# Kernel optimization log

Hardware: AMD Instinct MI355X
Metric: run time of the kernel (lower is better)

The kernel has to match this reference:

```python
import jax, jax.numpy as jnp
import numpy as np

B, L, E, H, D, OUT = 4, 2048, 1024, 8, 128, 1024


def setup_inputs() -> dict:
    key = jax.random.key(0)
    ks = jax.random.split(key, 6)
    stdv = 1.0 / np.sqrt(D)
    return {
        "k": jax.random.normal(ks[0], (B, L, E), dtype=jnp.float32),
        "q": jax.random.normal(ks[1], (B, L, E), dtype=jnp.float32),
        "w_kx": jax.random.uniform(ks[2], (H, E, D), minval=-stdv, maxval=stdv, dtype=jnp.float32),
        "w_qx": jax.random.uniform(ks[3], (H, E, D), minval=-stdv, maxval=stdv, dtype=jnp.float32),
        "proj_w": jax.random.normal(ks[4], (OUT, H * D), dtype=jnp.float32) * 0.02,
        "proj_b": jnp.zeros((OUT,), dtype=jnp.float32),
        "flag": False,
    }


def reference(k, q, w_kx, w_qx, proj_w, proj_b, flag):
    # Per-head sigmoid projections, vectorized over heads (original loops over heads).
    d = w_kx.shape[-1]
    kx = jax.nn.sigmoid(jnp.einsum('ble,hed->bhld', k, w_kx))  # [B,H,Lk,D]
    if flag:
        # flag==True: q is used directly (already hidden_dim-sized), shared across heads
        qx = jnp.broadcast_to(q[:, None], (q.shape[0], kx.shape[1], q.shape[1], q.shape[2]))
    else:
        qx = jax.nn.sigmoid(jnp.einsum('bqe,hed->bhqd', q, w_qx))  # [B,H,Lq,D]
    # scaled dot-product score + softmax over key axis
    score = jnp.einsum('bhqd,bhkd->bhqk', qx, kx) * (1.0 / jnp.sqrt(jnp.asarray(d, kx.dtype)))
    attn = jax.nn.softmax(score, axis=-1)
    out = jnp.einsum('bhqk,bhkd->bhqd', attn, kx)  # [B,H,Lq,D]
    # concat heads along feature dim, then linear projection (dropout p=0 -> identity)
    b, h, lq, _ = out.shape
    out = out.transpose(0, 2, 1, 3).reshape(b, lq, h * d)
    return out @ proj_w.T + proj_b
```

## Files before the change

### kernel.cpp

```cpp
#include <hip/hip_runtime.h>

#define BB 4
#define LL 2048
#define EE 1024
#define HH 8
#define DD 128
#define OO 1024
#define MM (BB*LL)
#define ND (HH*DD)

#define QBLK 128
#define KVBLK 64
#define NT (LL / KVBLK)

#define C2 0.12751920678739807f

typedef __bf16 bf16;
typedef unsigned short u16;
typedef __bf16 bf16x8 __attribute__((ext_vector_type(8)));
typedef __bf16 bf16x4 __attribute__((ext_vector_type(4)));
typedef float  f32x4  __attribute__((ext_vector_type(4)));

__device__ __forceinline__ void gl16(const bf16* g, bf16* l) {
#if __has_builtin(__builtin_amdgcn_global_load_lds)
    __builtin_amdgcn_global_load_lds((const __attribute__((address_space(1))) char*)g,
                                     (__attribute__((address_space(3))) char*)l, 16, 0, 0);
#else
    *(bf16x8*)l = *(const bf16x8*)g;
#endif
}

__device__ __forceinline__ bf16x8 cvt8(const float* s) {
    float4 f0 = *(const float4*)s;
    float4 f1 = *(const float4*)(s + 4);
    bf16x8 v;
    v[0] = (bf16)f0.x; v[1] = (bf16)f0.y; v[2] = (bf16)f0.z; v[3] = (bf16)f0.w;
    v[4] = (bf16)f1.x; v[5] = (bf16)f1.y; v[6] = (bf16)f1.z; v[7] = (bf16)f1.w;
    return v;
}

__global__ void detect_kernel(const u16* __restrict__ data, int* __restrict__ mode) {
    if (threadIdx.x == 0 && blockIdx.x == 0) {
        int cnt = 0;
        for (int i = 0; i < 512; i++) {
            int e = (data[i] >> 7) & 0xFF;
            if (e >= 117 && e <= 132) cnt++;
        }
        *mode = (cnt > 400) ? 1 : 0;
    }
}

__global__ __launch_bounds__(256) void fill_kernel(float* __restrict__ out, float v, int n) {
    int i = blockIdx.x * 256 + threadIdx.x;
    if (i < n) out[i] = v;
}

__global__ __launch_bounds__(256) void wtrans_kernel(const void* __restrict__ in0,
                                                     const void* __restrict__ in1,
                                                     bf16* __restrict__ outT0,
                                                     bf16* __restrict__ outT1,
                                                     const int* __restrict__ mode) {
    const void* in = blockIdx.y ? in1 : in0;
    bf16* outT = blockIdx.y ? outT1 : outT0;
    int idx = blockIdx.x * 256 + threadIdx.x;
    int i4 = idx * 4;
    int h = i4 >> 17;
    int rem = i4 & 131071;
    int e = rem >> 7;
    int d = rem & 127;
    size_t ob = ((size_t)h * DD + d) * EE + e;
    if (*mode) {
        bf16x4 v = *(const bf16x4*)((const bf16*)in + i4);
        outT[ob]          = v[0];
        outT[ob + EE]     = v[1];
        outT[ob + 2 * EE] = v[2];
        outT[ob + 3 * EE] = v[3];
    } else {
        float4 v = *(const float4*)((const float*)in + i4);
        outT[ob]          = (bf16)v.x;
        outT[ob + EE]     = (bf16)v.y;
        outT[ob + 2 * EE] = (bf16)v.z;
        outT[ob + 3 * EE] = (bf16)v.w;
    }
}

__global__ __launch_bounds__(256) void gemm_kernel(const void* __restrict__ A0,
                                                   const void* __restrict__ A1,
                                                   const void* __restrict__ BT0,
                                                   const void* __restrict__ BT1,
                                                   bf16* __restrict__ outBF0,
                                                   bf16* __restrict__ outBF1,
                                                   bf16* __restrict__ outT,
                                                   float* __restrict__ outF,
                                                   const void* __restrict__ PB,
                                                   const int* __restrict__ mode,
                                                   const int epi) {
    __shared__ __align__(16) bf16 As[128 * 64];
    __shared__ __align__(16) bf16 Bs[128 * 64];
    const int md = *mode;
    const int aBf = (epi == 2) ? 1 : md;
    const int bBf = (epi == 2) ? md : 1;
    const int t = threadIdx.x;
    const int w = t >> 6, l = t & 63;
    const int lr = l & 15, lg = l >> 4;
    const int wr = w >> 1, wc = w & 1;
    const int o = blockIdx.x + (blockIdx.y << 3);
    const int half = (epi == 3) ? (o >> 9) : 0;
    const int oo = o & 511;
    const int mt = (oo & 7) * 8 + ((oo >> 3) & 7);
    const int ntile = oo >> 6;
    const int m0 = mt * 128, n0 = ntile * 128;
    const void* A = half ? A1 : A0;
    const void* BT = half ? BT1 : BT0;

    f32x4 acc[4][4];
    const f32x4 zero = {0.f, 0.f, 0.f, 0.f};
#pragma unroll
    for (int i = 0; i < 4; i++)
#pragma unroll
        for (int j = 0; j < 4; j++) acc[i][j] = zero;

    for (int kt = 0; kt < 16; ++kt) {
        const int k0 = kt * 64;
        __syncthreads();
        if (aBf) {
#pragma unroll
            for (int p = 0; p < 4; p++) {
                const int id = p * 256 + t;
                const int row = id >> 3;
                const int c = (id & 7) ^ (row & 7);
                gl16((const bf16*)A + (size_t)(m0 + row) * 1024 + k0 + c * 8,
                     As + (p * 256 + w * 64) * 8);
            }
        } else {
#pragma unroll
            for (int p = 0; p < 4; p++) {
                const int id = p * 256 + t;
                const int row = id >> 3;
                const int cc = id & 7;
                bf16x8 v = cvt8((const float*)A + (size_t)(m0 + row) * 1024 + k0 + cc * 8);
                *(bf16x8*)(As + row * 64 + ((cc ^ (row & 7)) << 3)) = v;
            }
        }
        if (bBf) {
#pragma unroll
            for (int p = 0; p < 4; p++) {
                const int id = p * 256 + t;
                const int row = id >> 3;
                const int c = (id & 7) ^ (row & 7);
                gl16((const bf16*)BT + (size_t)(n0 + row) * 1024 + k0 + c * 8,
                     Bs + (p * 256 + w * 64) * 8);
            }
        } else {
#pragma unroll
            for (int p = 0; p < 4; p++) {
                const int id = p * 256 + t;
                const int row = id >> 3;
                const int cc = id & 7;
                bf16x8 v = cvt8((const float*)BT + (size_t)(n0 + row) * 1024 + k0 + cc * 8);
                *(bf16x8*)(Bs + row * 64 + ((cc ^ (row & 7)) << 3)) = v;
            }
        }
        __syncthreads();
        bf16x8 af[4][2], bg[4][2];
#pragma unroll
        for (int i = 0; i < 4; i++) {
            const int ar = wr * 64 + i * 16 + lr;
#pragma unroll
            for (int ks = 0; ks < 2; ks++)
                af[i][ks] = *(const bf16x8*)(As + ar * 64 + (((ks * 4 + lg) ^ (ar & 7)) << 3));
        }
#pragma unroll
        for (int j = 0; j < 4; j++) {
            const int br = wc * 64 + j * 16 + lr;
#pragma unroll
            for (int ks = 0; ks < 2; ks++)
                bg[j][ks] = *(const bf16x8*)(Bs + br * 64 + (((ks * 4 + lg) ^ (br & 7)) << 3));
        }
#pragma unroll
        for (int i = 0; i < 4; i++)
#pragma unroll
            for (int j = 0; j < 4; j++) {
                acc[i][j] = __builtin_amdgcn_mfma_f32_16x16x32_bf16(af[i][0], bg[j][0], acc[i][j], 0, 0, 0);
                acc[i][j] = __builtin_amdgcn_mfma_f32_16x16x32_bf16(af[i][1], bg[j][1], acc[i][j], 0, 0, 0);
            }
    }

    if (epi == 3) {
        bf16* outBF = half ? outBF1 : outBF0;
        const float mulf = half ? C2 : 1.0f;
        const int b_idx = m0 >> 11;
        const int h = n0 >> 7;
#pragma unroll
        for (int i = 0; i < 4; i++) {
#pragma unroll
            for (int j = 0; j < 4; j++) {
                const int gr = m0 + wr * 64 + i * 16 + lg * 4;
                const int gc = n0 + wc * 64 + j * 16 + lr;
                float s0 = mulf / (1.0f + __expf(-acc[i][j][0]));
                float s1 = mulf / (1.0f + __expf(-acc[i][j][1]));
                float s2 = mulf / (1.0f + __expf(-acc[i][j][2]));
                float s3 = mulf / (1.0f + __expf(-acc[i][j][3]));
                outBF[(size_t)gr * ND + gc]           = (bf16)s0;
                outBF[(size_t)(gr + 1) * ND + gc]     = (bf16)s1;
                outBF[(size_t)(gr + 2) * ND + gc]     = (bf16)s2;
                outBF[(size_t)(gr + 3) * ND + gc]     = (bf16)s3;
                if (!half) {
                    bf16x4 pk;
                    pk[0] = (bf16)s0; pk[1] = (bf16)s1; pk[2] = (bf16)s2; pk[3] = (bf16)s3;
                    const int d = gc & 127;
                    const int lrow = gr & 2047;
                    *(bf16x4*)(outT + (((size_t)(h * BB + b_idx)) * DD + d) * LL + lrow) = pk;
                }
            }
        }
    } else {
#pragma unroll
        for (int j = 0; j < 4; j++) {
            const int gc = n0 + wc * 64 + j * 16 + lr;
            const float bias = md ? (float)((const bf16*)PB)[gc] : ((const float*)PB)[gc];
#pragma unroll
            for (int i = 0; i < 4; i++) {
                const int gr = m0 + wr * 64 + i * 16 + lg * 4;
#pragma unroll
                for (int reg = 0; reg < 4; reg++)
                    outF[(size_t)(gr + reg) * OO + gc] = acc[i][j][reg] + bias;
            }
        }
    }
}

__global__ __launch_bounds__(512, 4) void attn_kernel(const bf16* __restrict__ QX,
                                                      const bf16* __restrict__ KX,
                                                      const bf16* __restrict__ KXT,
                                                      bf16* __restrict__ AO) {
    __shared__ __align__(16) bf16 Kl[2][KVBLK * 128];
    __shared__ __align__(16) bf16 Vt[2][128 * KVBLK];
    __shared__ __align__(16) bf16 Pl[8][16 * 64];
    const int t = threadIdx.x;
    const int w = t >> 6, l = t & 63;
    const int lr = l & 15, lg = l >> 4;
    const int bid = blockIdx.x;
    const int orig = (bid & 7) * 64 + (bid >> 3);
    const int bh = orig >> 4;
    const int h = bh & 7, b = bh >> 3;
    const int q0 = (orig & 15) * QBLK;
    const bf16* qxh = QX + (size_t)(b * LL) * ND + h * DD;
    const bf16* kxh = KX + (size_t)(b * LL) * ND + h * DD;
    const bf16* kxt = KXT + ((size_t)(h * BB + b)) * DD * LL;

    const int kid1 = 512 + t;
    const int krow0 = t >> 4,    kcc0 = t & 15;
    const int krow1 = kid1 >> 4, kcc1 = kid1 & 15;
    const int vrow0 = t >> 3,    vcc0 = t & 7;
    const int vrow1 = kid1 >> 3, vcc1 = kid1 & 7;
    const bf16* kp0 = kxh + (size_t)krow0 * ND + kcc0 * 8;
    const bf16* kp1 = kxh + (size_t)krow1 * ND + kcc1 * 8;
    const bf16* vp0 = kxt + (size_t)vrow0 * LL + vcc0 * 8;
    const bf16* vp1 = kxt + (size_t)vrow1 * LL + vcc1 * 8;
    const int kw0 = krow0 * 128 + ((kcc0 ^ (krow0 & 15)) << 3);
    const int kw1 = krow1 * 128 + ((kcc1 ^ (krow1 & 15)) << 3);
    const int vw0 = vrow0 * 64 + ((vcc0 ^ (vrow0 & 7)) << 3);
    const int vw1 = vrow1 * 64 + ((vcc1 ^ (vrow1 & 7)) << 3);

    bf16x8 qf[4];
    const int qrow = q0 + w * 16 + lr;
#pragma unroll
    for (int s = 0; s < 4; s++)
        qf[s] = *(const bf16x8*)(qxh + (size_t)qrow * ND + s * 32 + lg * 8);

    bf16x8 rk0 = *(const bf16x8*)(kp0);
    bf16x8 rk1 = *(const bf16x8*)(kp1);
    bf16x8 rv0 = *(const bf16x8*)(vp0);
    bf16x8 rv1 = *(const bf16x8*)(vp1);
    *(bf16x8*)(Kl[0] + kw0) = rk0;
    *(bf16x8*)(Kl[0] + kw1) = rk1;
    *(bf16x8*)(Vt[0] + vw0) = rv0;
    *(bf16x8*)(Vt[0] + vw1) = rv1;
    rk0 = *(const bf16x8*)(kp0 + (size_t)KVBLK * ND);
    rk1 = *(const bf16x8*)(kp1 + (size_t)KVBLK * ND);
    rv0 = *(const bf16x8*)(vp0 + KVBLK);
    rv1 = *(const bf16x8*)(vp1 + KVBLK);
    __syncthreads();

    f32x4 oacc[8];
    const f32x4 zero = {0.f, 0.f, 0.f, 0.f};
#pragma unroll
    for (int n = 0; n < 8; n++) oacc[n] = zero;
    float psum = 0.f;

    for (int kt = 0; kt < NT; ++kt) {
        const int cur = kt & 1;
        if (kt + 1 < NT) {
            *(bf16x8*)(Kl[cur ^ 1] + kw0) = rk0;
            *(bf16x8*)(Kl[cur ^ 1] + kw1) = rk1;
            *(bf16x8*)(Vt[cur ^ 1] + vw0) = rv0;
            *(bf16x8*)(Vt[cur ^ 1] + vw1) = rv1;
            if (kt + 2 < NT) {
                const size_t ko = (size_t)(kt + 2) * KVBLK * ND;
                const int vo = (kt + 2) * KVBLK;
                rk0 = *(const bf16x8*)(kp0 + ko);
                rk1 = *(const bf16x8*)(kp1 + ko);
                rv0 = *(const bf16x8*)(vp0 + vo);
                rv1 = *(const bf16x8*)(vp1 + vo);
            }
        }
        const bf16* KlC = Kl[cur];
        const bf16* VtC = Vt[cur];

        f32x4 sa[4];
        __builtin_amdgcn_s_setprio(1);
#pragma unroll
        for (int n = 0; n < 4; n++) {
            sa[n] = zero;
#pragma unroll
            for (int ks = 0; ks < 4; ks++) {
                int arow = n * 16 + lr;
                bf16x8 kb = *(const bf16x8*)(KlC + arow * 128 + ((((ks * 4 + lg) ^ (arow & 15))) << 3));
                sa[n] = __builtin_amdgcn_mfma_f32_16x16x32_bf16(kb, qf[ks], sa[n], 0, 0, 0);
            }
        }
        __builtin_amdgcn_s_setprio(0);
#pragma unroll
        for (int n = 0; n < 4; n++) {
            bf16x4 pk;
#pragma unroll
            for (int j = 0; j < 4; j++) {
                float p = exp2f(sa[n][j]);
                psum += p;
                pk[j] = (bf16)p;
            }
            const int chunk = (2 * n + (lg >> 1)) ^ (lr & 7);
            *(bf16x4*)(Pl[w] + lr * 64 + chunk * 8 + (lg & 1) * 4) = pk;
        }
        asm volatile("s_waitcnt lgkmcnt(0)" ::: "memory");
        __builtin_amdgcn_sched_barrier(0);
        bf16x8 pb0 = *(const bf16x8*)(Pl[w] + lr * 64 + (((lg ^ (lr & 7))) << 3));
        bf16x8 pb1 = *(const bf16x8*)(Pl[w] + lr * 64 + ((((4 + lg) ^ (lr & 7))) << 3));
        __builtin_amdgcn_s_setprio(1);
#pragma unroll
        for (int n = 0; n < 8; n++) {
            int vrow = n * 16 + lr;
            bf16x8 vb0 = *(const bf16x8*)(VtC + vrow * 64 + (((lg ^ (vrow & 7))) << 3));
            oacc[n] = __builtin_amdgcn_mfma_f32_16x16x32_bf16(vb0, pb0, oacc[n], 0, 0, 0);
            bf16x8 vb1 = *(const bf16x8*)(VtC + vrow * 64 + ((((4 + lg) ^ (vrow & 7))) << 3));
            oacc[n] = __builtin_amdgcn_mfma_f32_16x16x32_bf16(vb1, pb1, oacc[n], 0, 0, 0);
        }
        __builtin_amdgcn_s_setprio(0);
        __syncthreads();
    }
    float tot = psum;
    tot += __shfl_xor(tot, 16);
    tot += __shfl_xor(tot, 32);
    const float linv = 1.0f / tot;
    const int arow = b * LL + q0 + w * 16 + lr;
    bf16* aoRow = AO + (size_t)arow * ND + h * DD;
#pragma unroll
    for (int n = 0; n < 8; n++) {
        bf16x4 o;
#pragma unroll
        for (int reg = 0; reg < 4; reg++) o[reg] = (bf16)(oacc[n][reg] * linv);
        *(bf16x4*)(aoRow + n * 16 + lg * 4) = o;
    }
}

extern "C" void kernel_launch(void* const* d_in, const int* in_sizes, int n_in,
                              void* d_out, int out_size, void* d_ws, size_t ws_size,
                              hipStream_t stream) {
    (void)in_sizes; (void)n_in;
    float* out = (float*)d_out;

    const size_t NEED = ((size_t)(2 + 2 + 16 + 16 + 16 + 16) << 20) + 256;
    if (ws_size < NEED) {
        hipLaunchKernelGGL(fill_kernel, dim3((out_size + 255) / 256), dim3(256), 0, stream,
                           out, (float)(ws_size >> 20), out_size);
        return;
    }

    int* mode = (int*)d_ws;
    bf16* base = (bf16*)((char*)d_ws + 256);
    bf16* wkT = base;
    bf16* wqT = wkT + (size_t)HH * DD * EE;
    bf16* kx  = wqT + (size_t)HH * DD * EE;
    bf16* qx  = kx  + (size_t)MM * ND;
    bf16* kxT = qx  + (size_t)MM * ND;
    bf16* ao  = kxT + (size_t)HH * MM * DD;

    hipLaunchKernelGGL(detect_kernel, dim3(1), dim3(64), 0, stream, (const u16*)d_in[0], mode);
    hipLaunchKernelGGL(wtrans_kernel, dim3(HH * EE * DD / 4 / 256, 2), dim3(256), 0, stream,
                       d_in[2], d_in[3], wkT, wqT, mode);
    hipLaunchKernelGGL(gemm_kernel, dim3(8, 128), dim3(256), 0, stream,
                       d_in[0], d_in[1], wkT, wqT, kx, qx, kxT,
                       (float*)nullptr, (const void*)nullptr, mode, 3);
    hipLaunchKernelGGL(attn_kernel, dim3(512), dim3(512), 0, stream, qx, kx, kxT, ao);
    hipLaunchKernelGGL(gemm_kernel, dim3(8, 64), dim3(256), 0, stream,
                       ao, (const void*)nullptr, d_in[4], (const void*)nullptr,
                       (bf16*)nullptr, (bf16*)nullptr, (bf16*)nullptr, out, d_in[5], mode, 2);
}
```

Before: 199.4 us.

## Halve attention query block to 64 rows and single-buffer K/V in LDS

The attention kernel now processes 64 query rows per block with 4 waves instead of 128 rows with 8, doubling the grid to 1024 blocks. The K/V LDS staging drops double buffering in favor of a single buffer with register prefetch and two barriers per tile, and the P scratch swizzle is changed to a 4-element granularity. The aim is to cut LDS use per block and raise occupancy. In exchange, each K/V tile is reloaded by twice as many blocks and the extra barrier exposes more synchronization.

Result: slower. 249.3 us (+25.1%).

```diff
diff --git a/kernel.cpp b/kernel.cpp
--- a/kernel.cpp
+++ b/kernel.cpp
@@ -9,7 +9,7 @@
 #define MM (BB*LL)
 #define ND (HH*DD)
 
-#define QBLK 128
+#define QBLK 64
 #define KVBLK 64
 #define NT (LL / KVBLK)
 
@@ -230,38 +230,38 @@
     }
 }
 
-__global__ __launch_bounds__(512, 4) void attn_kernel(const bf16* __restrict__ QX,
+__global__ __launch_bounds__(256, 4) void attn_kernel(const bf16* __restrict__ QX,
                                                       const bf16* __restrict__ KX,
                                                       const bf16* __restrict__ KXT,
                                                       bf16* __restrict__ AO) {
-    __shared__ __align__(16) bf16 Kl[2][KVBLK * 128];
-    __shared__ __align__(16) bf16 Vt[2][128 * KVBLK];
-    __shared__ __align__(16) bf16 Pl[8][16 * 64];
+    __shared__ __align__(16) bf16 Kl[KVBLK * 128];
+    __shared__ __align__(16) bf16 Vt[128 * KVBLK];
+    __shared__ __align__(16) bf16 Pl[4][16 * 64];
     const int t = threadIdx.x;
     const int w = t >> 6, l = t & 63;
     const int lr = l & 15, lg = l >> 4;
     const int bid = blockIdx.x;
-    const int orig = (bid & 7) * 64 + (bid >> 3);
-    const int bh = orig >> 4;
+    const int orig = (bid & 7) * 128 + (bid >> 3);
+    const int bh = orig >> 5;
     const int h = bh & 7, b = bh >> 3;
-    const int q0 = (orig & 15) * QBLK;
+    const int q0 = (orig & 31) * QBLK;
     const bf16* qxh = QX + (size_t)(b * LL) * ND + h * DD;
     const bf16* kxh = KX + (size_t)(b * LL) * ND + h * DD;
     const bf16* kxt = KXT + ((size_t)(h * BB + b)) * DD * LL;
 
-    const int kid1 = 512 + t;
-    const int krow0 = t >> 4,    kcc0 = t & 15;
-    const int krow1 = kid1 >> 4, kcc1 = kid1 & 15;
-    const int vrow0 = t >> 3,    vcc0 = t & 7;
-    const int vrow1 = kid1 >> 3, vcc1 = kid1 & 7;
-    const bf16* kp0 = kxh + (size_t)krow0 * ND + kcc0 * 8;
-    const bf16* kp1 = kxh + (size_t)krow1 * ND + kcc1 * 8;
-    const bf16* vp0 = kxt + (size_t)vrow0 * LL + vcc0 * 8;
-    const bf16* vp1 = kxt + (size_t)vrow1 * LL + vcc1 * 8;
-    const int kw0 = krow0 * 128 + ((kcc0 ^ (krow0 & 15)) << 3);
-    const int kw1 = krow1 * 128 + ((kcc1 ^ (krow1 & 15)) << 3);
-    const int vw0 = vrow0 * 64 + ((vcc0 ^ (vrow0 & 7)) << 3);
-    const int vw1 = vrow1 * 64 + ((vcc1 ^ (vrow1 & 7)) << 3);
+    const bf16* kpK[4];
+    const bf16* kpV[4];
+    int kw[4], vw[4];
+#pragma unroll
+    for (int p = 0; p < 4; p++) {
+        const int id = p * 256 + t;
+        const int krow = id >> 4, kcc = id & 15;
+        kpK[p] = kxh + (size_t)krow * ND + kcc * 8;
+        kw[p] = krow * 128 + ((kcc ^ (krow & 15)) << 3);
+        const int vrow = id >> 3, vcc = id & 7;
+        kpV[p] = kxt + (size_t)vrow * LL + vcc * 8;
+        vw[p] = vrow * 64 + ((vcc ^ (vrow & 7)) << 3);
+    }
 
     bf16x8 qf[4];
     const int qrow = q0 + w * 16 + lr;
@@ -269,19 +269,12 @@
     for (int s = 0; s < 4; s++)
         qf[s] = *(const bf16x8*)(qxh + (size_t)qrow * ND + s * 32 + lg * 8);
 
-    bf16x8 rk0 = *(const bf16x8*)(kp0);
-    bf16x8 rk1 = *(const bf16x8*)(kp1);
-    bf16x8 rv0 = *(const bf16x8*)(vp0);
-    bf16x8 rv1 = *(const bf16x8*)(vp1);
-    *(bf16x8*)(Kl[0] + kw0) = rk0;
-    *(bf16x8*)(Kl[0] + kw1) = rk1;
-    *(bf16x8*)(Vt[0] + vw0) = rv0;
-    *(bf16x8*)(Vt[0] + vw1) = rv1;
-    rk0 = *(const bf16x8*)(kp0 + (size_t)KVBLK * ND);
-    rk1 = *(const bf16x8*)(kp1 + (size_t)KVBLK * ND);
-    rv0 = *(const bf16x8*)(vp0 + KVBLK);
-    rv1 = *(const bf16x8*)(vp1 + KVBLK);
-    __syncthreads();
+    bf16x8 rk[4], rv[4];
+#pragma unroll
+    for (int p = 0; p < 4; p++) {
+        rk[p] = *(const bf16x8*)(kpK[p]);
+        rv[p] = *(const bf16x8*)(kpV[p]);
+    }
 
     f32x4 oacc[8];
     const f32x4 zero = {0.f, 0.f, 0.f, 0.f};
@@ -290,23 +283,22 @@
     float psum = 0.f;
 
     for (int kt = 0; kt < NT; ++kt) {
-        const int cur = kt & 1;
+        __syncthreads();
+#pragma unroll
+        for (int p = 0; p < 4; p++) {
+            *(bf16x8*)(Kl + kw[p]) = rk[p];
+            *(bf16x8*)(Vt + vw[p]) = rv[p];
+        }
         if (kt + 1 < NT) {
-            *(bf16x8*)(Kl[cur ^ 1] + kw0) = rk0;
-            *(bf16x8*)(Kl[cur ^ 1] + kw1) = rk1;
-            *(bf16x8*)(Vt[cur ^ 1] + vw0) = rv0;
-            *(bf16x8*)(Vt[cur ^ 1] + vw1) = rv1;
-            if (kt + 2 < NT) {
-                const size_t ko = (size_t)(kt + 2) * KVBLK * ND;
-                const int vo = (kt + 2) * KVBLK;
-                rk0 = *(const bf16x8*)(kp0 + ko);
-                rk1 = *(const bf16x8*)(kp1 + ko);
-                rv0 = *(const bf16x8*)(vp0 + vo);
-                rv1 = *(const bf16x8*)(vp1 + vo);
-            }
-        }
-        const bf16* KlC = Kl[cur];
-        const bf16* VtC = Vt[cur];
+            const size_t ko = (size_t)(kt + 1) * KVBLK * ND;
+            const int vo = (kt + 1) * KVBLK;
+#pragma unroll
+            for (int p = 0; p < 4; p++) {
+                rk[p] = *(const bf16x8*)(kpK[p] + ko);
+                rv[p] = *(const bf16x8*)(kpV[p] + vo);
+            }
+        }
+        __syncthreads();
 
         f32x4 sa[4];
         __builtin_amdgcn_s_setprio(1);
@@ -316,7 +308,7 @@
 #pragma unroll
             for (int ks = 0; ks < 4; ks++) {
                 int arow = n * 16 + lr;
-                bf16x8 kb = *(const bf16x8*)(KlC + arow * 128 + ((((ks * 4 + lg) ^ (arow & 15))) << 3));
+                bf16x8 kb = *(const bf16x8*)(Kl + arow * 128 + ((((ks * 4 + lg) ^ (arow & 15))) << 3));
                 sa[n] = __builtin_amdgcn_mfma_f32_16x16x32_bf16(kb, qf[ks], sa[n], 0, 0, 0);
             }
         }
@@ -330,24 +322,23 @@
                 psum += p;
                 pk[j] = (bf16)p;
             }
-            const int chunk = (2 * n + (lg >> 1)) ^ (lr & 7);
-            *(bf16x4*)(Pl[w] + lr * 64 + chunk * 8 + (lg & 1) * 4) = pk;
+            const int pphys = (4 * n + lg) ^ (lr & 14);
+            *(bf16x4*)(Pl[w] + lr * 64 + pphys * 4) = pk;
         }
         asm volatile("s_waitcnt lgkmcnt(0)" ::: "memory");
         __builtin_amdgcn_sched_barrier(0);
-        bf16x8 pb0 = *(const bf16x8*)(Pl[w] + lr * 64 + (((lg ^ (lr & 7))) << 3));
-        bf16x8 pb1 = *(const bf16x8*)(Pl[w] + lr * 64 + ((((4 + lg) ^ (lr & 7))) << 3));
+        bf16x8 pb0 = *(const bf16x8*)(Pl[w] + lr * 64 + (((2 * lg) ^ (lr & 14)) << 2));
+        bf16x8 pb1 = *(const bf16x8*)(Pl[w] + lr * 64 + (((8 + 2 * lg) ^ (lr & 14)) << 2));
         __builtin_amdgcn_s_setprio(1);
 #pragma unroll
         for (int n = 0; n < 8; n++) {
             int vrow = n * 16 + lr;
-            bf16x8 vb0 = *(const bf16x8*)(VtC + vrow * 64 + (((lg ^ (vrow & 7))) << 3));
+            bf16x8 vb0 = *(const bf16x8*)(Vt + vrow * 64 + (((lg ^ (vrow & 7))) << 3));
             oacc[n] = __builtin_amdgcn_mfma_f32_16x16x32_bf16(vb0, pb0, oacc[n], 0, 0, 0);
-            bf16x8 vb1 = *(const bf16x8*)(VtC + vrow * 64 + ((((4 + lg) ^ (vrow & 7))) << 3));
+            bf16x8 vb1 = *(const bf16x8*)(Vt + vrow * 64 + ((((4 + lg) ^ (vrow & 7))) << 3));
             oacc[n] = __builtin_amdgcn_mfma_f32_16x16x32_bf16(vb1, pb1, oacc[n], 0, 0, 0);
         }
         __builtin_amdgcn_s_setprio(0);
-        __syncthreads();
     }
     float tot = psum;
     tot += __shfl_xor(tot, 16);
@@ -392,7 +383,7 @@
     hipLaunchKernelGGL(gemm_kernel, dim3(8, 128), dim3(256), 0, stream,
                        d_in[0], d_in[1], wkT, wqT, kx, qx, kxT,
                        (float*)nullptr, (const void*)nullptr, mode, 3);
-    hipLaunchKernelGGL(attn_kernel, dim3(512), dim3(512), 0, stream, qx, kx, kxT, ao);
+    hipLaunchKernelGGL(attn_kernel, dim3(1024), dim3(256), 0, stream, qx, kx, kxT, ao);
     hipLaunchKernelGGL(gemm_kernel, dim3(8, 64), dim3(256), 0, stream,
                        ao, (const void*)nullptr, d_in[4], (const void*)nullptr,
                        (bf16*)nullptr, (bf16*)nullptr, (bf16*)nullptr, out, d_in[5], mode, 2);
```
